# Kernel optimization log

Hardware: AMD Instinct MI355X
Metric: run time of the kernel (lower is better)

The kernel has to match this reference:

```python
import jax, jax.numpy as jnp
import numpy as np

N0, N1, N2, N3 = 524288, 262144, 65536, 8192
E0, E1, E2 = 2621440, 655360, 81920
D_IN, D_H, D_OUT = 256, 256, 64


def setup_inputs() -> dict:
    key = jax.random.key(0)
    ks = jax.random.split(key, 16)
    s = 0.02
    inp = {
        "x": jax.random.normal(ks[0], (N0, D_IN), dtype=jnp.float32),
        "src0": jax.random.randint(ks[1], (E0,), 0, N0, dtype=jnp.int32),
        "dst0": jax.random.randint(ks[2], (E0,), 0, N1, dtype=jnp.int32),
        "src1": jax.random.randint(ks[3], (E1,), 0, N1, dtype=jnp.int32),
        "dst1": jax.random.randint(ks[4], (E1,), 0, N2, dtype=jnp.int32),
        "src2": jax.random.randint(ks[5], (E2,), 0, N2, dtype=jnp.int32),
        "dst2": jax.random.randint(ks[6], (E2,), 0, N3, dtype=jnp.int32),
        "nd0": N1, "nd1": N2, "nd2": N3,
        "Wfc": jax.random.normal(ks[7], (D_IN, D_H), dtype=jnp.float32) * s,
        "bfc": jnp.zeros((D_H,), dtype=jnp.float32),
        "Ws0": jax.random.normal(ks[8], (D_H, D_H), dtype=jnp.float32) * s,
        "Wn0": jax.random.normal(ks[9], (D_H, D_H), dtype=jnp.float32) * s,
        "b0": jnp.zeros((D_H,), dtype=jnp.float32),
        "Ws1": jax.random.normal(ks[10], (D_H, D_H), dtype=jnp.float32) * s,
        "Wn1": jax.random.normal(ks[11], (D_H, D_H), dtype=jnp.float32) * s,
        "b1": jnp.zeros((D_H,), dtype=jnp.float32),
        "Ws2": jax.random.normal(ks[12], (D_H, D_OUT), dtype=jnp.float32) * s,
        "Wn2": jax.random.normal(ks[13], (D_H, D_OUT), dtype=jnp.float32) * s,
        "b2": jnp.zeros((D_OUT,), dtype=jnp.float32),
    }
    return inp


def sage_conv(h, src, dst, n_dst, Ws, Wn, b):
    # DGL SAGEConv 'mean': out = h_dst @ W_self + mean_neigh(h_src) @ W_neigh + b
    h_dst = h[:n_dst]
    msg = jnp.take(h, src, axis=0)                    # [E, d] gather
    agg = jax.ops.segment_sum(msg, dst, num_segments=n_dst)
    cnt = jax.ops.segment_sum(jnp.ones((dst.shape[0],), h.dtype), dst, num_segments=n_dst)
    mean = agg / jnp.maximum(cnt, 1.0)[:, None]
    return h_dst @ Ws + mean @ Wn + b


def reference(x, src0, dst0, src1, dst1, src2, dst2, nd0, nd1, nd2,
              Wfc, bfc, Ws0, Wn0, b0, Ws1, Wn1, b1, Ws2, Wn2, b2):
    h = jax.nn.relu(x @ Wfc + bfc)                    # input projection (dropout=0 -> identity)
    h = jax.nn.relu(sage_conv(h, src0, dst0, nd0, Ws0, Wn0, b0))
    h = jax.nn.relu(sage_conv(h, src1, dst1, nd1, Ws1, Wn1, b1))
    h = sage_conv(h, src2, dst2, nd2, Ws2, Wn2, b2)   # no activation on final layer
    return h
```

## Files before the change

### kernel.cpp

```cpp
#include <hip/hip_runtime.h>

constexpr int N0c = 524288, N1c = 262144, N2c = 65536, N3c = 8192;

typedef __attribute__((ext_vector_type(8))) short   bf16x8;
typedef __attribute__((ext_vector_type(4))) float   f32x4;
typedef __attribute__((ext_vector_type(4))) unsigned short u16x4;
typedef __attribute__((ext_vector_type(8))) unsigned short u16x8;

__device__ inline unsigned short f2bf(float f) {
    union { float f; unsigned u; } v; v.f = f;
    unsigned r = v.u + 0x7FFF + ((v.u >> 16) & 1);
    return (unsigned short)(r >> 16);
}
__device__ inline float bf2f(unsigned short u) {
    union { unsigned u; float f; } v; v.u = ((unsigned)u) << 16;
    return v.f;
}

__device__ inline void glds16(const void* g, void* l) {
    __builtin_amdgcn_global_load_lds(
        (const __attribute__((address_space(1))) unsigned int*)g,
        (__attribute__((address_space(3))) unsigned int*)l, 16, 0, 0);
}

__global__ __launch_bounds__(256)
void wconv_k(const float* __restrict__ W, unsigned short* __restrict__ Wt, int K, int N)
{
    const int i = blockIdx.x * 256 + threadIdx.x;
    if (i >= K * N) return;
    const int k = i / N, n = i % N;
    Wt[n * K + k] = f2bf(W[i]);
}

__device__ inline bf16x8 pack_bf8(const float* p) {
    const f32x4 u = *(const f32x4*)p;
    const f32x4 v = *(const f32x4*)(p + 4);
    bf16x8 t;
    #pragma unroll
    for (int j = 0; j < 4; ++j) {
        t[j]     = (short)f2bf(u[j]);
        t[j + 4] = (short)f2bf(v[j]);
    }
    return t;
}

template<int NT, int KC, bool DUAL, bool RELU, bool A_F32, bool OUT_BF16>
__global__ __launch_bounds__(512, 2)
void gemm2(const void* __restrict__ A1v, const void* __restrict__ A2v,
           const unsigned short* __restrict__ Wt1,
           const unsigned short* __restrict__ Wt2,
           const float* __restrict__ bias, void* __restrict__ Cv)
{
    constexpr int N     = NT * 16;
    constexpr int PH    = 256 / KC;
    constexpr int SLOTS = KC / 8;
    constexpr int GPM   = N * SLOTS;
    constexpr int TOTG  = GPM * (DUAL ? 2 : 1);
    static_assert(TOTG == 4096, "LDS sizing");
    __shared__ unsigned short Bs[TOTG * 8];

    const int t    = threadIdx.x;
    const int lane = t & 63;
    const int wv   = t >> 6;
    const int col  = lane & 15;
    const int kg   = lane >> 4;
    const int swz  = (col & 7) << 3;
    const long row0 = (long)blockIdx.x * 128 + wv * 16;

    const unsigned short* A1h = (const unsigned short*)A1v;
    const float*          A1f = (const float*)A1v;
    const unsigned short* A2h = (const unsigned short*)A2v;

    f32x4 acc[NT];
    #pragma unroll
    for (int nt = 0; nt < NT; ++nt) acc[nt] = (f32x4){0.f, 0.f, 0.f, 0.f};

    const long ar = (row0 + col) * 256;

    for (int kh = 0; kh < PH; ++kh) {
        if (kh) __syncthreads();
        #pragma unroll
        for (int it = 0; it < TOTG / 512; ++it) {
            const int g  = it * 512 + t;
            const int m  = DUAL ? (g / GPM) : 0;
            const int gm = DUAL ? (g % GPM) : g;
            const int n  = gm / SLOTS;
            const int s  = gm % SLOTS;
            const int ss = s ^ (n & 7);
            const unsigned short* srcb =
                (m ? Wt2 : Wt1) + n * 256 + kh * KC + ss * 8;
            glds16(srcb, &Bs[(it * 512 + wv * 64) * 8]);
        }
        __syncthreads();

        #pragma unroll
        for (int k0 = 0; k0 < KC; k0 += 32) {
            const int kx = (k0 + kg * 8) ^ swz;
            const long ac = ar + kh * KC + k0 + kg * 8;
            bf16x8 a1, a2;
            if constexpr (A_F32) a1 = pack_bf8(&A1f[ac]);
            else                 a1 = *(const bf16x8*)&A1h[ac];
            if constexpr (DUAL)  a2 = *(const bf16x8*)&A2h[ac];
            #pragma unroll
            for (int nt = 0; nt < NT; ++nt) {
                const bf16x8 b1 = *(const bf16x8*)&Bs[(nt * 16 + col) * KC + kx];
                acc[nt] = __builtin_amdgcn_mfma_f32_16x16x32_bf16(a1, b1, acc[nt], 0, 0, 0);
                if constexpr (DUAL) {
                    const bf16x8 b2 = *(const bf16x8*)&Bs[GPM * 8 + (nt * 16 + col) * KC + kx];
                    acc[nt] = __builtin_amdgcn_mfma_f32_16x16x32_bf16(a2, b2, acc[nt], 0, 0, 0);
                }
            }
        }
    }

    #pragma unroll
    for (int nt = 0; nt < NT; ++nt) {
        const int c = nt * 16 + col;
        const float bb = bias[c];
        #pragma unroll
        for (int rr = 0; rr < 4; ++rr) {
            const long row = row0 + kg * 4 + rr;
            float o = acc[nt][rr] + bb;
            if constexpr (RELU) o = fmaxf(o, 0.f);
            if constexpr (OUT_BF16)
                ((unsigned short*)Cv)[row * N + c] = f2bf(o);
            else
                ((float*)Cv)[row * N + c] = o;
        }
    }
}


__global__ __launch_bounds__(256)
void hist_k(const int* __restrict__ dst, int* __restrict__ hist, int E)
{
    const int i = blockIdx.x * 256 + threadIdx.x;
    if (i < E) atomicAdd(&hist[dst[i]], 1);
}

__global__ __launch_bounds__(256)
void scan1_k(const int* __restrict__ hist, int* __restrict__ offs,
             int* __restrict__ bsum, int n)
{
    __shared__ int sm[256];
    const int t = threadIdx.x;
    const int base = blockIdx.x * 1024 + t * 4;
    int4 v = make_int4(0, 0, 0, 0);
    if (base < n) v = *(const int4*)&hist[base];
    const int s = v.x + v.y + v.z + v.w;
    int val = s;
    sm[t] = val; __syncthreads();
    #pragma unroll
    for (int off = 1; off < 256; off <<= 1) {
        const int add = (t >= off) ? sm[t - off] : 0;
        __syncthreads();
        val += add;
        sm[t] = val;
        __syncthreads();
    }
    const int excl = val - s;
    if (base < n) {
        offs[base]     = excl;
        offs[base + 1] = excl + v.x;
        offs[base + 2] = excl + v.x + v.y;
        offs[base + 3] = excl + v.x + v.y + v.z;
    }
    if (t == 255) bsum[blockIdx.x] = val;
}

__global__ __launch_bounds__(256)
void scan2_k(int* __restrict__ bsum, int nb)
{
    __shared__ int sm[256];
    const int t = threadIdx.x;
    const int s = (t < nb) ? bsum[t] : 0;
    int val = s;
    sm[t] = val; __syncthreads();
    #pragma unroll
    for (int off = 1; off < 256; off <<= 1) {
        const int add = (t >= off) ? sm[t - off] : 0;
        __syncthreads();
        val += add;
        sm[t] = val;
        __syncthreads();
    }
    if (t < nb) bsum[t] = val - s;
}

__global__ __launch_bounds__(256)
void scan3_k(int* __restrict__ offs, const int* __restrict__ bsum)
{
    const int i = blockIdx.x * 256 + threadIdx.x;
    offs[i] += bsum[i >> 10];
}

__global__ __launch_bounds__(256)
void fill_k(const int* __restrict__ src, const int* __restrict__ dst,
            const int* __restrict__ offs, int* __restrict__ hist,
            int* __restrict__ ssrc, int E)
{
    const int i = blockIdx.x * 256 + threadIdx.x;
    if (i < E) {
        const int d = dst[i];
        const int p = atomicAdd(&hist[d], -1) - 1;
        ssrc[offs[d] + p] = src[i];
    }
}

__global__ __launch_bounds__(256)
void agg_k(const unsigned short* __restrict__ h, const int* __restrict__ ssrc,
           const int* __restrict__ offs, unsigned short* __restrict__ agg,
           int n, int E)
{
    const int w    = blockIdx.x * 4 + (threadIdx.x >> 6);
    const int lane = threadIdx.x & 63;
    if (w >= n) return;
    const int beg = offs[w];
    const int end = (w == n - 1) ? E : offs[w + 1];
    const int hf  = lane >> 5;
    const int co  = (lane & 31) * 8;

    float acc[8] = {0.f, 0.f, 0.f, 0.f, 0.f, 0.f, 0.f, 0.f};

    for (int j = beg; j < end; j += 16) {
        u16x8 v[8];
        bool  ok[8];
        #pragma unroll
        for (int q = 0; q < 8; ++q) {
            const int e  = j + 2 * q + hf;
            ok[q] = (e < end);
            const int es = ok[q] ? e : (end - 1);
            v[q] = *(const u16x8*)&h[(size_t)ssrc[es] * 256 + co];
        }
        #pragma unroll
        for (int q = 0; q < 8; ++q)
            #pragma unroll
            for (int c = 0; c < 8; ++c)
                acc[c] += ok[q] ? bf2f(v[q][c]) : 0.0f;
    }

    #pragma unroll
    for (int c = 0; c < 8; ++c) acc[c] += __shfl_xor(acc[c], 32);

    if (hf == 0) {
        const float inv = 1.0f / fmaxf((float)(end - beg), 1.0f);
        u16x8 o;
        #pragma unroll
        for (int c = 0; c < 8; ++c) o[c] = f2bf(acc[c] * inv);
        *(u16x8*)&agg[(size_t)w * 256 + co] = o;
    }
}

static void build_and_aggregate(const unsigned short* h, const int* src, const int* dst,
                                int n, int E, int* hist, int* offs, int* bsum,
                                int* ssrc, unsigned short* agg, hipStream_t stream)
{
    const dim3 blk(256);
    hipMemsetAsync(hist, 0, (size_t)n * 4, stream);
    hist_k<<<dim3((E + 255) / 256), blk, 0, stream>>>(dst, hist, E);
    scan1_k<<<dim3(n / 1024), blk, 0, stream>>>(hist, offs, bsum, n);
    scan2_k<<<dim3(1), blk, 0, stream>>>(bsum, n / 1024);
    scan3_k<<<dim3(n / 256), blk, 0, stream>>>(offs, bsum);
    fill_k<<<dim3((E + 255) / 256), blk, 0, stream>>>(src, dst, offs, hist, ssrc, E);
    agg_k<<<dim3(n / 4), blk, 0, stream>>>(h, ssrc, offs, agg, n, E);
}

extern "C" void kernel_launch(void* const* d_in, const int* in_sizes, int n_in,
                              void* d_out, int out_size, void* d_ws, size_t ws_size,
                              hipStream_t stream)
{
    const float* x    = (const float*)d_in[0];
    const int*   src0 = (const int*)d_in[1];
    const int*   dst0 = (const int*)d_in[2];
    const int*   src1 = (const int*)d_in[3];
    const int*   dst1 = (const int*)d_in[4];
    const int*   src2 = (const int*)d_in[5];
    const int*   dst2 = (const int*)d_in[6];
    const float* Wfc  = (const float*)d_in[10];
    const float* bfc  = (const float*)d_in[11];
    const float* Ws0  = (const float*)d_in[12];
    const float* Wn0  = (const float*)d_in[13];
    const float* b0   = (const float*)d_in[14];
    const float* Ws1  = (const float*)d_in[15];
    const float* Wn1  = (const float*)d_in[16];
    const float* b1   = (const float*)d_in[17];
    const float* Ws2  = (const float*)d_in[18];
    const float* Wn2  = (const float*)d_in[19];
    const float* b2   = (const float*)d_in[20];
    const int E0 = in_sizes[1], E1 = in_sizes[3], E2 = in_sizes[5];

    char* ws = (char*)d_ws;
    unsigned short* h0   = (unsigned short*)ws;
    unsigned short* h1   = (unsigned short*)(ws + (256ULL << 20));
    unsigned short* h2   = (unsigned short*)(ws + (384ULL << 20));
    unsigned short* agg  = (unsigned short*)(ws + (416ULL << 20));
    unsigned short* Wt   = (unsigned short*)(ws + (544ULL << 20));
    int*            hist = (int*)(ws + (545ULL << 20));
    int*            offs = (int*)(ws + (546ULL << 20));
    int*            bsum = (int*)(ws + (547ULL << 20));
    int*            ssrc = (int*)(ws + (548ULL << 20));

    unsigned short* wfc = Wt;
    unsigned short* ws0 = Wt + 65536;
    unsigned short* wn0 = Wt + 131072;
    unsigned short* ws1 = Wt + 196608;
    unsigned short* wn1 = Wt + 262144;
    unsigned short* ws2 = Wt + 327680;
    unsigned short* wn2 = Wt + 344064;

    const dim3 blk(256);

    wconv_k<<<dim3(256), blk, 0, stream>>>(Wfc, wfc, 256, 256);
    wconv_k<<<dim3(256), blk, 0, stream>>>(Ws0, ws0, 256, 256);
    wconv_k<<<dim3(256), blk, 0, stream>>>(Wn0, wn0, 256, 256);
    wconv_k<<<dim3(256), blk, 0, stream>>>(Ws1, ws1, 256, 256);
    wconv_k<<<dim3(256), blk, 0, stream>>>(Wn1, wn1, 256, 256);
    wconv_k<<<dim3(64),  blk, 0, stream>>>(Ws2, ws2, 256, 64);
    wconv_k<<<dim3(64),  blk, 0, stream>>>(Wn2, wn2, 256, 64);

    gemm2<16, 128, false, true, true, true><<<dim3(N0c / 128), dim3(512), 0, stream>>>(
        x, nullptr, wfc, nullptr, bfc, h0);

    build_and_aggregate(h0, src0, dst0, N1c, E0, hist, offs, bsum, ssrc, agg, stream);
    gemm2<16, 64, true, true, false, true><<<dim3(N1c / 128), dim3(512), 0, stream>>>(
        h0, agg, ws0, wn0, b0, h1);

    build_and_aggregate(h1, src1, dst1, N2c, E1, hist, offs, bsum, ssrc, agg, stream);
    gemm2<16, 64, true, true, false, true><<<dim3(N2c / 128), dim3(512), 0, stream>>>(
        h1, agg, ws1, wn1, b1, h2);

    build_and_aggregate(h2, src2, dst2, N3c, E2, hist, offs, bsum, ssrc, agg, stream);
    gemm2<4, 256, true, false, false, false><<<dim3(N3c / 128), dim3(512), 0, stream>>>(
        h2, agg, ws2, wn2, b2, (float*)d_out);
}
```

Baseline: 984.5 us.

## Batch CSR construction for all three layers and merge weight conversions

Builds the CSR for all three edge lists in a single concatenated pass: one memset, one histogram, one three-stage scan over the combined destination range, and one fill, with a sentinel offset so aggregation no longer special-cases the last row. The seven weight-conversion launches become one kernel. This removes about twenty small kernel launches and their serialization. In exchange the graph work now happens before the first GEMM, and the scan and workspace layout grow to cover all layers.

```diff
diff --git a/kernel.cpp b/kernel.cpp
--- a/kernel.cpp
+++ b/kernel.cpp
@@ -1,10 +1,10 @@
 #include <hip/hip_runtime.h>
 
 constexpr int N0c = 524288, N1c = 262144, N2c = 65536, N3c = 8192;
+constexpr int NTOT = N1c + N2c + N3c;
 
 typedef __attribute__((ext_vector_type(8))) short   bf16x8;
 typedef __attribute__((ext_vector_type(4))) float   f32x4;
-typedef __attribute__((ext_vector_type(4))) unsigned short u16x4;
 typedef __attribute__((ext_vector_type(8))) unsigned short u16x8;
 
 __device__ inline unsigned short f2bf(float f) {
@@ -23,13 +23,21 @@
         (__attribute__((address_space(3))) unsigned int*)l, 16, 0, 0);
 }
 
-__global__ __launch_bounds__(256)
-void wconv_k(const float* __restrict__ W, unsigned short* __restrict__ Wt, int K, int N)
-{
-    const int i = blockIdx.x * 256 + threadIdx.x;
-    if (i >= K * N) return;
-    const int k = i / N, n = i % N;
-    Wt[n * K + k] = f2bf(W[i]);
+struct WPack { const float* w[7]; unsigned short* o[7]; };
+
+__global__ __launch_bounds__(256)
+void wconv_all(WPack p)
+{
+    const int idx = blockIdx.x * 256 + threadIdx.x;
+    int widx, off, N;
+    if (idx < 327680) { widx = idx >> 16; off = idx & 65535; N = 256; }
+    else {
+        const int r = idx - 327680;
+        widx = 5 + (r >> 14); off = r & 16383; N = 64;
+        if (widx > 6) return;
+    }
+    const int k = off / N, n = off % N;
+    p.o[widx][n * 256 + k] = f2bf(p.w[widx][off]);
 }
 
 __device__ inline bf16x8 pack_bf8(const float* p) {
@@ -130,12 +138,23 @@
     }
 }
 
-
-__global__ __launch_bounds__(256)
-void hist_k(const int* __restrict__ dst, int* __restrict__ hist, int E)
+struct CsrArgs {
+    const int* src0; const int* dst0;
+    const int* src1; const int* dst1;
+    const int* src2; const int* dst2;
+    int e0, e01, etot;
+};
+
+__global__ __launch_bounds__(256)
+void hist_all(CsrArgs a, int* __restrict__ hist)
 {
     const int i = blockIdx.x * 256 + threadIdx.x;
-    if (i < E) atomicAdd(&hist[dst[i]], 1);
+    if (i >= a.etot) return;
+    const int* dstp; int e, hb;
+    if (i < a.e0)       { dstp = a.dst0; e = i;         hb = 0; }
+    else if (i < a.e01) { dstp = a.dst1; e = i - a.e0;  hb = N1c; }
+    else                { dstp = a.dst2; e = i - a.e01; hb = N1c + N2c; }
+    atomicAdd(&hist[hb + dstp[e]], 1);
 }
 
 __global__ __launch_bounds__(256)
@@ -168,16 +187,16 @@
     if (t == 255) bsum[blockIdx.x] = val;
 }
 
-__global__ __launch_bounds__(256)
+__global__ __launch_bounds__(512)
 void scan2_k(int* __restrict__ bsum, int nb)
 {
-    __shared__ int sm[256];
+    __shared__ int sm[512];
     const int t = threadIdx.x;
     const int s = (t < nb) ? bsum[t] : 0;
     int val = s;
     sm[t] = val; __syncthreads();
     #pragma unroll
-    for (int off = 1; off < 256; off <<= 1) {
+    for (int off = 1; off < 512; off <<= 1) {
         const int add = (t >= off) ? sm[t - off] : 0;
         __syncthreads();
         val += add;
@@ -188,35 +207,37 @@
 }
 
 __global__ __launch_bounds__(256)
-void scan3_k(int* __restrict__ offs, const int* __restrict__ bsum)
+void scan3_k(int* __restrict__ offs, const int* __restrict__ bsum, int etot)
 {
     const int i = blockIdx.x * 256 + threadIdx.x;
     offs[i] += bsum[i >> 10];
-}
-
-__global__ __launch_bounds__(256)
-void fill_k(const int* __restrict__ src, const int* __restrict__ dst,
-            const int* __restrict__ offs, int* __restrict__ hist,
-            int* __restrict__ ssrc, int E)
+    if (i == 0) offs[NTOT] = etot;
+}
+
+__global__ __launch_bounds__(256)
+void fill_all(CsrArgs a, const int* __restrict__ offs, int* __restrict__ hist,
+              int* __restrict__ ssrc)
 {
     const int i = blockIdx.x * 256 + threadIdx.x;
-    if (i < E) {
-        const int d = dst[i];
-        const int p = atomicAdd(&hist[d], -1) - 1;
-        ssrc[offs[d] + p] = src[i];
-    }
+    if (i >= a.etot) return;
+    const int* dstp; const int* srcp; int e, hb;
+    if (i < a.e0)       { dstp = a.dst0; srcp = a.src0; e = i;         hb = 0; }
+    else if (i < a.e01) { dstp = a.dst1; srcp = a.src1; e = i - a.e0;  hb = N1c; }
+    else                { dstp = a.dst2; srcp = a.src2; e = i - a.e01; hb = N1c + N2c; }
+    const int g = hb + dstp[e];
+    const int p = atomicAdd(&hist[g], -1) - 1;
+    ssrc[offs[g] + p] = srcp[e];
 }
 
 __global__ __launch_bounds__(256)
 void agg_k(const unsigned short* __restrict__ h, const int* __restrict__ ssrc,
-           const int* __restrict__ offs, unsigned short* __restrict__ agg,
-           int n, int E)
+           const int* __restrict__ ob, unsigned short* __restrict__ agg, int n)
 {
     const int w    = blockIdx.x * 4 + (threadIdx.x >> 6);
     const int lane = threadIdx.x & 63;
     if (w >= n) return;
-    const int beg = offs[w];
-    const int end = (w == n - 1) ? E : offs[w + 1];
+    const int beg = ob[w];
+    const int end = ob[w + 1];
     const int hf  = lane >> 5;
     const int co  = (lane & 31) * 8;
 
@@ -249,20 +270,6 @@
         for (int c = 0; c < 8; ++c) o[c] = f2bf(acc[c] * inv);
         *(u16x8*)&agg[(size_t)w * 256 + co] = o;
     }
-}
-
-static void build_and_aggregate(const unsigned short* h, const int* src, const int* dst,
-                                int n, int E, int* hist, int* offs, int* bsum,
-                                int* ssrc, unsigned short* agg, hipStream_t stream)
-{
-    const dim3 blk(256);
-    hipMemsetAsync(hist, 0, (size_t)n * 4, stream);
-    hist_k<<<dim3((E + 255) / 256), blk, 0, stream>>>(dst, hist, E);
-    scan1_k<<<dim3(n / 1024), blk, 0, stream>>>(hist, offs, bsum, n);
-    scan2_k<<<dim3(1), blk, 0, stream>>>(bsum, n / 1024);
-    scan3_k<<<dim3(n / 256), blk, 0, stream>>>(offs, bsum);
-    fill_k<<<dim3((E + 255) / 256), blk, 0, stream>>>(src, dst, offs, hist, ssrc, E);
-    agg_k<<<dim3(n / 4), blk, 0, stream>>>(h, ssrc, offs, agg, n, E);
 }
 
 extern "C" void kernel_launch(void* const* d_in, const int* in_sizes, int n_in,
@@ -288,6 +295,7 @@
     const float* Wn2  = (const float*)d_in[19];
     const float* b2   = (const float*)d_in[20];
     const int E0 = in_sizes[1], E1 = in_sizes[3], E2 = in_sizes[5];
+    const int Etot = E0 + E1 + E2;
 
     char* ws = (char*)d_ws;
     unsigned short* h0   = (unsigned short*)ws;
@@ -296,9 +304,9 @@
     unsigned short* agg  = (unsigned short*)(ws + (416ULL << 20));
     unsigned short* Wt   = (unsigned short*)(ws + (544ULL << 20));
     int*            hist = (int*)(ws + (545ULL << 20));
-    int*            offs = (int*)(ws + (546ULL << 20));
-    int*            bsum = (int*)(ws + (547ULL << 20));
-    int*            ssrc = (int*)(ws + (548ULL << 20));
+    int*            offs = (int*)(ws + (547ULL << 20));
+    int*            bsum = (int*)(ws + (549ULL << 20));
+    int*            ssrc = (int*)(ws + (550ULL << 20));
 
     unsigned short* wfc = Wt;
     unsigned short* ws0 = Wt + 65536;
@@ -310,26 +318,36 @@
 
     const dim3 blk(256);
 
-    wconv_k<<<dim3(256), blk, 0, stream>>>(Wfc, wfc, 256, 256);
-    wconv_k<<<dim3(256), blk, 0, stream>>>(Ws0, ws0, 256, 256);
-    wconv_k<<<dim3(256), blk, 0, stream>>>(Wn0, wn0, 256, 256);
-    wconv_k<<<dim3(256), blk, 0, stream>>>(Ws1, ws1, 256, 256);
-    wconv_k<<<dim3(256), blk, 0, stream>>>(Wn1, wn1, 256, 256);
-    wconv_k<<<dim3(64),  blk, 0, stream>>>(Ws2, ws2, 256, 64);
-    wconv_k<<<dim3(64),  blk, 0, stream>>>(Wn2, wn2, 256, 64);
+    WPack wp;
+    wp.w[0] = Wfc; wp.w[1] = Ws0; wp.w[2] = Wn0; wp.w[3] = Ws1; wp.w[4] = Wn1;
+    wp.w[5] = Ws2; wp.w[6] = Wn2;
+    wp.o[0] = wfc; wp.o[1] = ws0; wp.o[2] = wn0; wp.o[3] = ws1; wp.o[4] = wn1;
+    wp.o[5] = ws2; wp.o[6] = wn2;
+    wconv_all<<<dim3(1408), blk, 0, stream>>>(wp);
+
+    CsrArgs ca;
+    ca.src0 = src0; ca.dst0 = dst0; ca.src1 = src1; ca.dst1 = dst1;
+    ca.src2 = src2; ca.dst2 = dst2;
+    ca.e0 = E0; ca.e01 = E0 + E1; ca.etot = Etot;
+    hipMemsetAsync(hist, 0, (size_t)NTOT * 4, stream);
+    hist_all<<<dim3((Etot + 255) / 256), blk, 0, stream>>>(ca, hist);
+    scan1_k<<<dim3(NTOT / 1024), blk, 0, stream>>>(hist, offs, bsum, NTOT);
+    scan2_k<<<dim3(1), dim3(512), 0, stream>>>(bsum, NTOT / 1024);
+    scan3_k<<<dim3(NTOT / 256), blk, 0, stream>>>(offs, bsum, Etot);
+    fill_all<<<dim3((Etot + 255) / 256), blk, 0, stream>>>(ca, offs, hist, ssrc);
 
     gemm2<16, 128, false, true, true, true><<<dim3(N0c / 128), dim3(512), 0, stream>>>(
         x, nullptr, wfc, nullptr, bfc, h0);
 
-    build_and_aggregate(h0, src0, dst0, N1c, E0, hist, offs, bsum, ssrc, agg, stream);
+    agg_k<<<dim3(N1c / 4), blk, 0, stream>>>(h0, ssrc, offs, agg, N1c);
     gemm2<16, 64, true, true, false, true><<<dim3(N1c / 128), dim3(512), 0, stream>>>(
         h0, agg, ws0, wn0, b0, h1);
 
-    build_and_aggregate(h1, src1, dst1, N2c, E1, hist, offs, bsum, ssrc, agg, stream);
+    agg_k<<<dim3(N2c / 4), blk, 0, stream>>>(h1, ssrc, offs + N1c, agg, N2c);
     gemm2<16, 64, true, true, false, true><<<dim3(N2c / 128), dim3(512), 0, stream>>>(
         h1, agg, ws1, wn1, b1, h2);
 
-    build_and_aggregate(h2, src2, dst2, N3c, E2, hist, offs, bsum, ssrc, agg, stream);
+    agg_k<<<dim3(N3c / 4), blk, 0, stream>>>(h2, ssrc, offs + N1c + N2c, agg, N3c);
     gemm2<4, 256, true, false, false, false><<<dim3(N3c / 128), dim3(512), 0, stream>>>(
         h2, agg, ws2, wn2, b2, (float*)d_out);
 }
```

Result: faster. 937.8 us (-4.7%).
